# Kernel optimization log

Hardware: AMD Instinct MI355X
Metric: run time of the kernel (lower is better)

Reference implementation:

```python
import jax, jax.numpy as jnp
import numpy as np

D_MODEL = 1024
H = 16
T = 1024
B = 8

def setup_inputs() -> dict:
    key = jax.random.key(0)
    k0, k1, k2, k3, k4 = jax.random.split(key, 5)
    return {
        "x": jax.random.normal(k0, (B, T, D_MODEL), dtype=jnp.float32),
        "Wq": jax.random.normal(k1, (D_MODEL, D_MODEL), dtype=jnp.float32),
        "Wk": jax.random.normal(k2, (D_MODEL, D_MODEL), dtype=jnp.float32),
        "Wv": jax.random.normal(k3, (D_MODEL, D_MODEL), dtype=jnp.float32),
        "Wp": jax.random.normal(k4, (D_MODEL, D_MODEL), dtype=jnp.float32),
    }

def reference(x, Wq, Wk, Wv, Wp):
    b, t, d = x.shape
    dh = d // H
    # projections
    q = (x @ Wq).reshape(b, t, H, dh)
    k = (x @ Wk).reshape(b, t, H, dh)
    v = (x @ Wv).reshape(b, t, H, dh)
    # [b, h, t, t] attention scores, scaled by sqrt(d_head)
    scores = jnp.einsum("bqhd,bkhd->bhqk", q, k) / jnp.sqrt(jnp.float32(dh))
    attn = jax.nn.softmax(scores, axis=-1)
    # [b, h, t, dh] -> [b, t, d]
    out = jnp.einsum("bhqk,bkhd->bqhd", attn, v).reshape(b, t, d)
    return out @ Wp
```

## Files before the change

kernel.cpp:

```cpp
#include <hip/hip_runtime.h>
#include <math.h>


typedef unsigned short u16;
typedef unsigned int u32;
typedef __bf16  bf16x8 __attribute__((ext_vector_type(8)));
typedef unsigned short u16x8 __attribute__((ext_vector_type(8)));
typedef unsigned short u16x4 __attribute__((ext_vector_type(4)));
typedef short s16x4 __attribute__((ext_vector_type(4)));
typedef unsigned int u32x2 __attribute__((ext_vector_type(2)));
typedef float f32x4 __attribute__((ext_vector_type(4)));

#define MFMA16(a,b,c) __builtin_amdgcn_mfma_f32_16x16x32_bf16((a),(b),(c),0,0,0)
#define MFMA16K16(a,b,c) __builtin_amdgcn_mfma_f32_16x16x16bf16_1k((a),(b),(c),0,0,0)

static __device__ __forceinline__ u16 f2b(float f){
  unsigned u = __builtin_bit_cast(unsigned, f);
  u += 0x7fffu + ((u >> 16) & 1u);
  return (u16)(u >> 16);
}
static __device__ __forceinline__ float b2f(u16 h){
  unsigned u = ((unsigned)h) << 16;
  return __builtin_bit_cast(float, u);
}
static __device__ __forceinline__ bf16x8 ldsfrag(const u16* p){
  return __builtin_bit_cast(bf16x8, *(const u16x8*)p);
}
static __device__ __forceinline__ u32 packhi(float fa, float fb){
  return __builtin_amdgcn_perm(__builtin_bit_cast(u32, fa),
                               __builtin_bit_cast(u32, fb), 0x07060302u);
}
static __device__ __forceinline__ void gld16(const void* g, void* l){
  __builtin_amdgcn_global_load_lds(
      (const __attribute__((address_space(1))) void*)g,
      (__attribute__((address_space(3))) void*)l, 16, 0, 0);
}


__global__ __launch_bounds__(256) void split_x_kernel(
    const float* __restrict__ x, u16* __restrict__ xh, u16* __restrict__ xl, int n)
{
  int i = (blockIdx.x * 256 + threadIdx.x) * 8;
  if (i >= n) return;
  float4 v0 = *(const float4*)(x + i);
  float4 v1 = *(const float4*)(x + i + 4);
  float vv[8] = {v0.x, v0.y, v0.z, v0.w, v1.x, v1.y, v1.z, v1.w};
  u16x8 hv, lv;
#pragma unroll
  for (int j = 0; j < 8; j++){
    u16 hb = f2b(vv[j]);
    hv[j] = hb;
    lv[j] = f2b(vv[j] - b2f(hb));
  }
  *(u16x8*)(xh + i) = hv;
  *(u16x8*)(xl + i) = lv;
}

__global__ __launch_bounds__(256) void transpose4_kernel(
    const float* __restrict__ Wq, const float* __restrict__ Wk,
    const float* __restrict__ Wv, const float* __restrict__ Wp,
    u16* __restrict__ qh_, u16* __restrict__ ql_,
    u16* __restrict__ kh_, u16* __restrict__ kl_,
    u16* __restrict__ vt_, u16* __restrict__ pt_)
{
  __shared__ float t[32][33];
  const int z = blockIdx.z;
  const float* W = (z == 0) ? Wq : (z == 1) ? Wk : (z == 2) ? Wv : Wp;
  u16* Th = (z == 0) ? qh_ : (z == 1) ? kh_ : (z == 2) ? vt_ : pt_;
  u16* Tl = (z == 0) ? ql_ : (z == 1) ? kl_ : nullptr;
  int n0 = blockIdx.x * 32, k0 = blockIdx.y * 32;
  int tx = threadIdx.x, ty = threadIdx.y;
#pragma unroll
  for (int i = 0; i < 4; i++){
    int k = k0 + ty + i * 8;
    t[ty + i * 8][tx] = W[(size_t)k * 1024 + n0 + tx];
  }
  __syncthreads();
#pragma unroll
  for (int i = 0; i < 4; i++){
    int n = n0 + ty + i * 8;
    float v = t[tx][ty + i * 8];
    u16 h = f2b(v);
    Th[(size_t)n * 1024 + k0 + tx] = h;
    if (Tl) Tl[(size_t)n * 1024 + k0 + tx] = f2b(v - b2f(h));
  }
}

template<int OUTMODE>
__global__ __launch_bounds__(256) void gemm_bt_kernel(
    const u16* __restrict__ A, const u16* __restrict__ Bt, void* __restrict__ Cv,
    int M, int N, int K)
{
  __shared__ __attribute__((aligned(16))) u16 lA[4096], lB[4096];
  const int tid = threadIdx.x, lane = tid & 63, wave = tid >> 6;
  const int quad = lane >> 4, l15 = lane & 15;
  const int row0 = blockIdx.x * 128, col0 = blockIdx.y * 128;
  const int wm = wave >> 1, wn = wave & 1;
  const int sr = lane >> 2, sc = (lane & 3) * 8;
  f32x4 acc[4][4];
#pragma unroll
  for (int mt = 0; mt < 4; mt++)
#pragma unroll
    for (int nt = 0; nt < 4; nt++) acc[mt][nt] = (f32x4)0.0f;

  for (int k0 = 0; k0 < K; k0 += 32){
#pragma unroll
    for (int i = 0; i < 2; i++){
      int c = wave * 2 + i;
      gld16(A  + (size_t)(row0 + c * 16 + sr) * K + k0 + sc, &lA[c * 512]);
      gld16(Bt + (size_t)(col0 + c * 16 + sr) * K + k0 + sc, &lB[c * 512]);
    }
    __syncthreads();
    bf16x8 a[4], b[4];
#pragma unroll
    for (int t = 0; t < 4; t++){
      a[t] = ldsfrag(&lA[(wm * 64 + t * 16 + l15) * 32 + quad * 8]);
      b[t] = ldsfrag(&lB[(wn * 64 + t * 16 + l15) * 32 + quad * 8]);
    }
#pragma unroll
    for (int mt = 0; mt < 4; mt++)
#pragma unroll
      for (int nt = 0; nt < 4; nt++)
        acc[mt][nt] = MFMA16(a[mt], b[nt], acc[mt][nt]);
    __syncthreads();
  }
  if (OUTMODE == 2){
#pragma unroll
    for (int mt = 0; mt < 4; mt++)
#pragma unroll
      for (int nt = 0; nt < 4; nt++){
        int row = row0 + wm * 64 + mt * 16 + quad * 4;
        int col = col0 + wn * 64 + nt * 16 + l15;
        int bb = row >> 10, tt = row & 1023;
        int hh = (col >> 6) & 15, d = col & 63;
        int bhI = bb * 16 + hh;
        int ktile = tt >> 7, fkt = (tt >> 4) & 7, qF = (tt >> 2) & 3;
        int nd = d >> 4, l15F = d & 15;
        size_t idx = ((((size_t)(bhI * 8 + ktile) * 8 + fkt) * 4 + nd) * 64
                      + qF * 16 + l15F) * 4;
        u16x4 vals;
#pragma unroll
        for (int r = 0; r < 4; r++) vals[r] = f2b(acc[mt][nt][r]);
        *(u16x4*)(((u16*)Cv) + idx) = vals;
      }
  } else {
#pragma unroll
    for (int mt = 0; mt < 4; mt++)
#pragma unroll
      for (int nt = 0; nt < 4; nt++)
#pragma unroll
        for (int r = 0; r < 4; r++){
          int row = row0 + wm * 64 + mt * 16 + quad * 4 + r;
          int col = col0 + wn * 64 + nt * 16 + l15;
          ((float*)Cv)[(size_t)row * N + col] = acc[mt][nt][r];
        }
  }
}

__global__ __launch_bounds__(512, 2) void gemm_qk_kernel(
    const u16* __restrict__ Ah, const u16* __restrict__ Al,
    const u16* __restrict__ Bh, const u16* __restrict__ Bl,
    u16* __restrict__ Qhf, u16* __restrict__ Qlf,
    u16* __restrict__ Khf, u16* __restrict__ Klf, int M, int N, int K)
{
  __shared__ __attribute__((aligned(16))) u16 sA[2][2][8192], sB[2][2][8192];
  const int tid = threadIdx.x, lane = tid & 63, wave = tid >> 6;
  const int quad = lane >> 4, l15 = lane & 15;
  const int wm = wave >> 2, wn = wave & 3;
  const int row0 = blockIdx.x * 256, col0 = blockIdx.y * 256;
  const int f0a = (wave & 3) | ((wave & 4) << 1);
  const int f0b = (wave & 1) | ((wave >> 1) << 2);
  const size_t fstride = (size_t)16 * K;
  const size_t abase = (size_t)(row0 + l15) * K + quad * 8;
  const size_t bbase = (size_t)(col0 + l15) * K + quad * 8;
  (void)M; (void)N;

  f32x4 acc[8][4];
#pragma unroll
  for (int mt = 0; mt < 8; mt++)
#pragma unroll
    for (int nt = 0; nt < 4; nt++) acc[mt][nt] = (f32x4)0.0f;

#define STAGE_G0(KK, NB) do {                                              \
    gld16(Ah + abase + (size_t)f0a * fstride + (KK), &sA[NB][0][f0a * 512]); \
    gld16(Al + abase + (size_t)f0a * fstride + (KK), &sA[NB][1][f0a * 512]); \
    gld16(Bh + bbase + (size_t)f0b * fstride + (KK), &sB[NB][0][f0b * 512]); \
    gld16(Bl + bbase + (size_t)f0b * fstride + (KK), &sB[NB][1][f0b * 512]); \
  } while (0)
#define STAGE_G1(KK, NB) do {                                                        \
    gld16(Bh + bbase + (size_t)(f0b + 2) * fstride + (KK), &sB[NB][0][(f0b + 2) * 512]); \
    gld16(Bl + bbase + (size_t)(f0b + 2) * fstride + (KK), &sB[NB][1][(f0b + 2) * 512]); \
  } while (0)
#define STAGE_G2(KK, NB) do {                                                        \
    gld16(Ah + abase + (size_t)(f0a + 4) * fstride + (KK), &sA[NB][0][(f0a + 4) * 512]); \
    gld16(Al + abase + (size_t)(f0a + 4) * fstride + (KK), &sA[NB][1][(f0a + 4) * 512]); \
  } while (0)
#define RD_A(B4, BUF) do {                                        \
    _Pragma("unroll")                                             \
    for (int i = 0; i < 4; i++){                                  \
      int fa = wm * 8 + (B4) + i;                                 \
      ahf[i] = ldsfrag(&sA[BUF][0][fa * 512 + lane * 8]);         \
      alf[i] = ldsfrag(&sA[BUF][1][fa * 512 + lane * 8]);         \
    } } while (0)
#define RD_B(B2, BUF) do {                                        \
    _Pragma("unroll")                                             \
    for (int j = 0; j < 2; j++){                                  \
      int fb = wn * 4 + (B2) + j;                                 \
      bhf[j] = ldsfrag(&sB[BUF][0][fb * 512 + lane * 8]);         \
      blf[j] = ldsfrag(&sB[BUF][1][fb * 512 + lane * 8]);         \
    } } while (0)
#define MM(M0, N0) do {                                                      \
    __builtin_amdgcn_s_setprio(1);                                           \
    _Pragma("unroll")                                                        \
    for (int i = 0; i < 4; i++)                                              \
      _Pragma("unroll")                                                      \
      for (int j = 0; j < 2; j++){                                           \
        acc[(M0) + i][(N0) + j] = MFMA16(alf[i], bhf[j], acc[(M0) + i][(N0) + j]); \
        acc[(M0) + i][(N0) + j] = MFMA16(ahf[i], blf[j], acc[(M0) + i][(N0) + j]); \
        acc[(M0) + i][(N0) + j] = MFMA16(ahf[i], bhf[j], acc[(M0) + i][(N0) + j]); \
      }                                                                      \
    __builtin_amdgcn_s_setprio(0);                                           \
  } while (0)
#define VMCNT4() asm volatile("s_waitcnt vmcnt(4)" ::: "memory")
#define VMCNT6() asm volatile("s_waitcnt vmcnt(6)" ::: "memory")
#define BARRIER() asm volatile("s_barrier" ::: "memory")

  const int NT = K >> 5;
  STAGE_G0(0, 0);
  STAGE_G1(0, 0);
  STAGE_G2(0, 0);

  bf16x8 ahf[4], alf[4], bhf[2], blf[2];
#pragma unroll 2
  for (int t = 0; t < NT; t++){
    const int buf = t & 1, nb = buf ^ 1;
    const int kn = ((t + 1) & (NT - 1)) * 32;
    VMCNT4();
    BARRIER();
    RD_A(0, buf);
    RD_B(0, buf);
    STAGE_G0(kn, nb);
    MM(0, 0);
    VMCNT6();
    BARRIER();
    RD_B(2, buf);
    STAGE_G1(kn, nb);
    MM(0, 2);
    VMCNT6();
    BARRIER();
    RD_A(4, buf);
    STAGE_G2(kn, nb);
    MM(4, 2);
    RD_B(0, buf);
    MM(4, 0);
  }
  asm volatile("s_waitcnt vmcnt(0)" ::: "memory");

#undef STAGE_G0
#undef STAGE_G1
#undef STAGE_G2
#undef RD_A
#undef RD_B
#undef MM
#undef VMCNT4
#undef VMCNT6
#undef BARRIER

  const bool isQ = (col0 < 1024);
#pragma unroll
  for (int mt = 0; mt < 8; mt++)
#pragma unroll
    for (int nt = 0; nt < 4; nt++)
#pragma unroll
      for (int r = 0; r < 4; r++){
        int row = row0 + wm * 128 + mt * 16 + quad * 4 + r;
        int col = col0 + wn * 64 + nt * 16 + l15;
        int bb = row >> 10, tt = row & 1023;
        int hh = (col >> 6) & 15, d = col & 63;
        int bhI = bb * 16 + hh;
        int kc = d >> 5, qF = (d >> 3) & 3, j = d & 7;
        float v = acc[mt][nt][r];
        u16 hi = f2b(v);
        u16 lo = f2b(v - b2f(hi));
        if (isQ){
          int qtile = tt >> 7, rr = tt & 127;
          int wv = rr >> 5, mtF = (rr >> 4) & 1, l15F = tt & 15;
          size_t idx = ((((size_t)(bhI * 8 + qtile) * 4 + wv) * 2 + mtF) * 2 + kc) * 512
                       + (qF * 16 + l15F) * 8 + j;
          Qhf[idx] = hi; Qlf[idx] = lo;
        } else {
          int ktile = tt >> 7, fkt = (tt >> 4) & 7, l15F = tt & 15;
          size_t idx = (((size_t)(bhI * 8 + ktile) * 8 + fkt) * 2 + kc) * 512
                       + (qF * 16 + l15F) * 8 + j;
          Khf[idx] = hi; Klf[idx] = lo;
        }
      }
}

__global__ __launch_bounds__(256, 2) void attn_kernel(
    const u16* __restrict__ Qhf, const u16* __restrict__ Qlf,
    const u16* __restrict__ Khf, const u16* __restrict__ Klf,
    const u16* __restrict__ Vf, u16* __restrict__ O)
{
  __shared__ __attribute__((aligned(16))) u16 lKh[2][4096], lKl[2][4096], lV[2][4096];
  const int tid = threadIdx.x, lane = tid & 63, wave = tid >> 6;
  const int quad = lane >> 4, l15 = lane & 15;
  const int qt = blockIdx.x >> 7, bh = blockIdx.x & 127;
  const int b = bh >> 4, h = bh & 15;
  const int q0 = qt * 256;
  const float BETA = 0.18033688011112042f;

  bf16x8 qh[2][2][2], ql[2][2][2];
  {
    u16* sh = &lKh[0][0];  u16* sl = &lKl[0][0];
#pragma unroll
    for (int g = 0; g < 2; g++){
      size_t qbase = ((size_t)((bh * 8 + 2 * qt + g) * 4 + wave)) * 2048 + lane * 8;
#pragma unroll
      for (int i = 0; i < 4; i++){
        gld16(Qhf + qbase + i * 512, sh + wave * 2048 + i * 512);
        gld16(Qlf + qbase + i * 512, sl + wave * 2048 + i * 512);
      }
      __syncthreads();
#pragma unroll
      for (int mt = 0; mt < 2; mt++)
#pragma unroll
        for (int kc = 0; kc < 2; kc++){
          int off = wave * 2048 + (mt * 2 + kc) * 512 + lane * 8;
          qh[g][mt][kc] = ldsfrag(sh + off);
          ql[g][mt][kc] = ldsfrag(sl + off);
        }
      __syncthreads();
    }
  }

  float m_i[2][2] = {{-3.0e38f, -3.0e38f}, {-3.0e38f, -3.0e38f}};
  float l_i[2][2] = {{0.0f, 0.0f}, {0.0f, 0.0f}};
  f32x4 o_acc[2][2][4];
#pragma unroll
  for (int g = 0; g < 2; g++)
#pragma unroll
    for (int mt = 0; mt < 2; mt++)
#pragma unroll
      for (int nd = 0; nd < 4; nd++) o_acc[g][mt][nd] = (f32x4)0.0f;

  const size_t pan = (size_t)bh * 65536;
#pragma unroll
  for (int i = 0; i < 2; i++){
    int c = wave * 2 + i;
    gld16(Khf + pan + c * 512 + lane * 8, &lKh[0][c * 512]);
    gld16(Klf + pan + c * 512 + lane * 8, &lKl[0][c * 512]);
    gld16(Vf  + pan + c * 512 + lane * 8, &lV [0][c * 512]);
  }

#pragma unroll 1
  for (int j = 0; j < 16; j++){
    const int cur = j & 1;
    __syncthreads();
    if (j < 15){
      size_t nb = pan + (size_t)(j + 1) * 4096;
      const int nxt = cur ^ 1;
#pragma unroll
      for (int i = 0; i < 2; i++){
        int c = wave * 2 + i;
        gld16(Khf + nb + c * 512 + lane * 8, &lKh[nxt][c * 512]);
        gld16(Klf + nb + c * 512 + lane * 8, &lKl[nxt][c * 512]);
        gld16(Vf  + nb + c * 512 + lane * 8, &lV [nxt][c * 512]);
      }
    }

#pragma unroll
    for (int g = 0; g < 2; g++){
      f32x4 s[2][4];
#pragma unroll
      for (int qt2 = 0; qt2 < 2; qt2++)
#pragma unroll
        for (int f4 = 0; f4 < 4; f4++) s[qt2][f4] = (f32x4)0.0f;
#pragma unroll
      for (int f4 = 0; f4 < 4; f4++){
        int aoff = f4 * 1024 + lane * 8;
        bf16x8 kh0 = ldsfrag(&lKh[cur][aoff]);
        bf16x8 kh1 = ldsfrag(&lKh[cur][aoff + 512]);
        bf16x8 kl0 = ldsfrag(&lKl[cur][aoff]);
        bf16x8 kl1 = ldsfrag(&lKl[cur][aoff + 512]);
        __builtin_amdgcn_s_setprio(1);
#pragma unroll
        for (int qt2 = 0; qt2 < 2; qt2++){
          s[qt2][f4] = MFMA16(kl0, qh[g][qt2][0], s[qt2][f4]);
          s[qt2][f4] = MFMA16(kl1, qh[g][qt2][1], s[qt2][f4]);
          s[qt2][f4] = MFMA16(kh0, ql[g][qt2][0], s[qt2][f4]);
          s[qt2][f4] = MFMA16(kh1, ql[g][qt2][1], s[qt2][f4]);
          s[qt2][f4] = MFMA16(kh0, qh[g][qt2][0], s[qt2][f4]);
          s[qt2][f4] = MFMA16(kh1, qh[g][qt2][1], s[qt2][f4]);
        }
        __builtin_amdgcn_s_setprio(0);
      }

      float alpha[2];
#pragma unroll
      for (int qt2 = 0; qt2 < 2; qt2++){
        f32x4 mv = s[qt2][0];
#pragma unroll
        for (int f4 = 1; f4 < 4; f4++){
          mv[0] = fmaxf(mv[0], s[qt2][f4][0]); mv[1] = fmaxf(mv[1], s[qt2][f4][1]);
          mv[2] = fmaxf(mv[2], s[qt2][f4][2]); mv[3] = fmaxf(mv[3], s[qt2][f4][3]);
        }
        float mx = fmaxf(fmaxf(mv[0], mv[1]), fmaxf(mv[2], mv[3]));
        mx = fmaxf(mx, __shfl_xor(mx, 16));
        mx = fmaxf(mx, __shfl_xor(mx, 32));
        float mn = fmaxf(m_i[g][qt2], mx);
        alpha[qt2] = __builtin_amdgcn_exp2f((m_i[g][qt2] - mn) * BETA);
        m_i[g][qt2] = mn;
        float mb = mn * BETA;
        f32x4 ps = (f32x4)0.0f;
#pragma unroll
        for (int f4 = 0; f4 < 4; f4++)
#pragma unroll
          for (int r = 0; r < 4; r++){
            float p = __builtin_amdgcn_exp2f(s[qt2][f4][r] * BETA - mb);
            s[qt2][f4][r] = p;
            ps[r] += p;
          }
        float rs = (ps[0] + ps[1]) + (ps[2] + ps[3]);
        rs += __shfl_xor(rs, 16);
        rs += __shfl_xor(rs, 32);
        l_i[g][qt2] = l_i[g][qt2] * alpha[qt2] + rs;
      }

#pragma unroll
      for (int mt = 0; mt < 2; mt++)
#pragma unroll
        for (int r = 0; r < 4; r++){
          float ar = __shfl(alpha[mt], quad * 4 + r);
#pragma unroll
          for (int nd = 0; nd < 4; nd++) o_acc[g][mt][nd][r] *= ar;
        }

#pragma unroll
      for (int f4 = 0; f4 < 4; f4++){
        s16x4 vb[4];
#pragma unroll
        for (int nd = 0; nd < 4; nd++)
          vb[nd] = __builtin_bit_cast(s16x4,
                     *(const u16x4*)&lV[cur][(f4 * 4 + nd) * 256 + lane * 4]);
        __builtin_amdgcn_s_setprio(1);
#pragma unroll
        for (int qt2 = 0; qt2 < 2; qt2++){
          u32x2 pd;
          pd[0] = packhi(s[qt2][f4][1], s[qt2][f4][0]);
          pd[1] = packhi(s[qt2][f4][3], s[qt2][f4][2]);
          s16x4 pa = __builtin_bit_cast(s16x4, pd);
#pragma unroll
          for (int nd = 0; nd < 4; nd++)
            o_acc[g][qt2][nd] = MFMA16K16(pa, vb[nd], o_acc[g][qt2][nd]);
        }
        __builtin_amdgcn_s_setprio(0);
      }
    }
  }

#pragma unroll
  for (int g = 0; g < 2; g++)
#pragma unroll
    for (int mt = 0; mt < 2; mt++)
#pragma unroll
      for (int r = 0; r < 4; r++){
        float lr = __shfl(l_i[g][mt], quad * 4 + r);
        float inv = 1.0f / lr;
        int t = q0 + g * 128 + wave * 32 + mt * 16 + quad * 4 + r;
        size_t rowoff = (size_t)(b * 1024 + t) * 1024 + h * 64;
#pragma unroll
        for (int nd = 0; nd < 4; nd++)
          O[rowoff + nd * 16 + l15] = f2b(o_acc[g][mt][nd][r] * inv);
      }
}

extern "C" void kernel_launch(void* const* d_in, const int* in_sizes, int n_in,
                              void* d_out, int out_size, void* d_ws, size_t ws_size,
                              hipStream_t stream)
{
  const float* x  = (const float*)d_in[0];
  const float* Wq = (const float*)d_in[1];
  const float* Wk = (const float*)d_in[2];
  const float* Wv = (const float*)d_in[3];
  const float* Wp = (const float*)d_in[4];
  float* out = (float*)d_out;
  char* ws = (char*)d_ws;
  const size_t MB = 1024 * 1024;
  u16* xh   = (u16*)(ws + 0);
  u16* xl   = (u16*)(ws + 16 * MB);
  u16* wqkh = (u16*)(ws + 32 * MB);
  u16* wqkl = (u16*)(ws + 36 * MB);
  u16* wvt  = (u16*)(ws + 40 * MB);
  u16* wpt  = (u16*)(ws + 42 * MB);
  u16* Qhf  = (u16*)(ws + 44 * MB);
  u16* Qlf  = (u16*)(ws + 60 * MB);
  u16* Khf  = (u16*)(ws + 76 * MB);
  u16* Klf  = (u16*)(ws + 92 * MB);
  u16* Vf   = (u16*)(ws + 108 * MB);
  u16* obuf = xh;
  (void)in_sizes; (void)n_in; (void)out_size; (void)ws_size;

  split_x_kernel<<<4096, 256, 0, stream>>>(x, xh, xl, 8 * 1024 * 1024);
  transpose4_kernel<<<dim3(32, 32, 4), dim3(32, 8), 0, stream>>>(
      Wq, Wk, Wv, Wp, wqkh, wqkl, wqkh + 1024 * 1024, wqkl + 1024 * 1024, wvt, wpt);
  gemm_qk_kernel<<<dim3(32, 8), 512, 0, stream>>>(xh, xl, wqkh, wqkl,
                                                  Qhf, Qlf, Khf, Klf, 8192, 2048, 1024);
  gemm_bt_kernel<2><<<dim3(64, 8), 256, 0, stream>>>(xh, wvt, (void*)Vf, 8192, 1024, 1024);
  attn_kernel<<<512, 256, 0, stream>>>(Qhf, Qlf, Khf, Klf, Vf, obuf);
  gemm_bt_kernel<0><<<dim3(64, 8), 256, 0, stream>>>(obuf, wpt, (void*)out, 8192, 1024, 1024);
}
```

Baseline: 334.8 us.

## Double-buffer GEMM LDS tiles and prefetch next K-slice during MFMA

The projection GEMM kernel now keeps two LDS buffers and issues global-to-LDS loads for the next K-slice before computing on the current one, replacing the two syncthreads per iteration with a single waitcnt plus barrier. The LDS layout changes to lane-major fragment order, so each lane reads its fragment contiguously. MFMA sections are wrapped in s_setprio to favour math issue. This doubles LDS use per block, which may lower occupancy, and the wrapped prefetch on the last iteration issues redundant loads.

```diff
diff --git a/kernel.cpp b/kernel.cpp
--- a/kernel.cpp
+++ b/kernel.cpp
@@ -91,39 +91,54 @@
     const u16* __restrict__ A, const u16* __restrict__ Bt, void* __restrict__ Cv,
     int M, int N, int K)
 {
-  __shared__ __attribute__((aligned(16))) u16 lA[4096], lB[4096];
+  __shared__ __attribute__((aligned(16))) u16 lA[2][4096], lB[2][4096];
   const int tid = threadIdx.x, lane = tid & 63, wave = tid >> 6;
   const int quad = lane >> 4, l15 = lane & 15;
   const int row0 = blockIdx.x * 128, col0 = blockIdx.y * 128;
   const int wm = wave >> 1, wn = wave & 1;
-  const int sr = lane >> 2, sc = (lane & 3) * 8;
+  const int c0 = wave * 2, c1 = wave * 2 + 1;
+  const size_t ar0 = (size_t)(row0 + c0 * 16 + l15) * K + quad * 8;
+  const size_t ar1 = (size_t)(row0 + c1 * 16 + l15) * K + quad * 8;
+  const size_t br0 = (size_t)(col0 + c0 * 16 + l15) * K + quad * 8;
+  const size_t br1 = (size_t)(col0 + c1 * 16 + l15) * K + quad * 8;
   f32x4 acc[4][4];
 #pragma unroll
   for (int mt = 0; mt < 4; mt++)
 #pragma unroll
     for (int nt = 0; nt < 4; nt++) acc[mt][nt] = (f32x4)0.0f;
 
-  for (int k0 = 0; k0 < K; k0 += 32){
-#pragma unroll
-    for (int i = 0; i < 2; i++){
-      int c = wave * 2 + i;
-      gld16(A  + (size_t)(row0 + c * 16 + sr) * K + k0 + sc, &lA[c * 512]);
-      gld16(Bt + (size_t)(col0 + c * 16 + sr) * K + k0 + sc, &lB[c * 512]);
+  const int NT = K >> 5;
+  gld16(A  + ar0, &lA[0][c0 * 512]);
+  gld16(A  + ar1, &lA[0][c1 * 512]);
+  gld16(Bt + br0, &lB[0][c0 * 512]);
+  gld16(Bt + br1, &lB[0][c1 * 512]);
+
+#pragma unroll 2
+  for (int t = 0; t < NT; t++){
+    const int buf = t & 1, nb = buf ^ 1;
+    const int kn = ((t + 1) & (NT - 1)) * 32;
+    asm volatile("s_waitcnt vmcnt(0)" ::: "memory");
+    asm volatile("s_barrier" ::: "memory");
+    gld16(A  + ar0 + kn, &lA[nb][c0 * 512]);
+    gld16(A  + ar1 + kn, &lA[nb][c1 * 512]);
+    gld16(Bt + br0 + kn, &lB[nb][c0 * 512]);
+    gld16(Bt + br1 + kn, &lB[nb][c1 * 512]);
+    bf16x8 a[4], b[4];
+#pragma unroll
+    for (int f = 0; f < 4; f++){
+      a[f] = ldsfrag(&lA[buf][(wm * 4 + f) * 512 + lane * 8]);
+      b[f] = ldsfrag(&lB[buf][(wn * 4 + f) * 512 + lane * 8]);
     }
-    __syncthreads();
-    bf16x8 a[4], b[4];
-#pragma unroll
-    for (int t = 0; t < 4; t++){
-      a[t] = ldsfrag(&lA[(wm * 64 + t * 16 + l15) * 32 + quad * 8]);
-      b[t] = ldsfrag(&lB[(wn * 64 + t * 16 + l15) * 32 + quad * 8]);
-    }
+    __builtin_amdgcn_s_setprio(1);
 #pragma unroll
     for (int mt = 0; mt < 4; mt++)
 #pragma unroll
       for (int nt = 0; nt < 4; nt++)
         acc[mt][nt] = MFMA16(a[mt], b[nt], acc[mt][nt]);
-    __syncthreads();
-  }
+    __builtin_amdgcn_s_setprio(0);
+  }
+  asm volatile("s_waitcnt vmcnt(0)" ::: "memory");
+
   if (OUTMODE == 2){
 #pragma unroll
     for (int mt = 0; mt < 4; mt++)
```

Result: slower. 349.6 us (+4.4%).

## Double-buffer gemm_bt with 128x256 tiles, async prefetch and MFMA priority

Applied to the files above, without the earlier changes.

Reworks the bf16 B-transposed GEMM used for the V projection and the output projection. The block tile grows to 128x256 with 512 threads. Global-to-LDS loads for the next 64-wide K slice go into a second LDS buffer while MFMAs run on the current one, synchronised with manual vmcnt waits and barriers in place of two __syncthreads per step. LDS now holds fragments in lane-contiguous order, and s_setprio raises wave priority around the MFMA bursts. The goal is to hide global load latency and halve barrier overhead, at the cost of about 96KB of LDS per block, which limits occupancy.

```diff
diff --git a/kernel.cpp b/kernel.cpp
--- a/kernel.cpp
+++ b/kernel.cpp
@@ -87,43 +87,66 @@
 }
 
 template<int OUTMODE>
-__global__ __launch_bounds__(256) void gemm_bt_kernel(
+__global__ __launch_bounds__(512, 2) void gemm_bt_kernel(
     const u16* __restrict__ A, const u16* __restrict__ Bt, void* __restrict__ Cv,
     int M, int N, int K)
 {
-  __shared__ __attribute__((aligned(16))) u16 lA[4096], lB[4096];
+  __shared__ __attribute__((aligned(16))) u16 sA[2][2][4096], sB[2][2][8192];
   const int tid = threadIdx.x, lane = tid & 63, wave = tid >> 6;
   const int quad = lane >> 4, l15 = lane & 15;
-  const int row0 = blockIdx.x * 128, col0 = blockIdx.y * 128;
-  const int wm = wave >> 1, wn = wave & 1;
-  const int sr = lane >> 2, sc = (lane & 3) * 8;
+  const int wm = wave >> 2, wn = wave & 3;
+  const int row0 = blockIdx.x * 128, col0 = blockIdx.y * 256;
+  const size_t abase  = (size_t)(row0 + wave * 16 + l15) * K + quad * 8;
+  const size_t bbase0 = (size_t)(col0 + (2 * wave) * 16 + l15) * K + quad * 8;
+  const size_t bbase1 = (size_t)(col0 + (2 * wave + 1) * 16 + l15) * K + quad * 8;
+  (void)M;
+
   f32x4 acc[4][4];
 #pragma unroll
   for (int mt = 0; mt < 4; mt++)
 #pragma unroll
     for (int nt = 0; nt < 4; nt++) acc[mt][nt] = (f32x4)0.0f;
 
-  for (int k0 = 0; k0 < K; k0 += 32){
-#pragma unroll
-    for (int i = 0; i < 2; i++){
-      int c = wave * 2 + i;
-      gld16(A  + (size_t)(row0 + c * 16 + sr) * K + k0 + sc, &lA[c * 512]);
-      gld16(Bt + (size_t)(col0 + c * 16 + sr) * K + k0 + sc, &lB[c * 512]);
-    }
-    __syncthreads();
-    bf16x8 a[4], b[4];
-#pragma unroll
-    for (int t = 0; t < 4; t++){
-      a[t] = ldsfrag(&lA[(wm * 64 + t * 16 + l15) * 32 + quad * 8]);
-      b[t] = ldsfrag(&lB[(wn * 64 + t * 16 + l15) * 32 + quad * 8]);
-    }
-#pragma unroll
-    for (int mt = 0; mt < 4; mt++)
-#pragma unroll
-      for (int nt = 0; nt < 4; nt++)
-        acc[mt][nt] = MFMA16(a[mt], b[nt], acc[mt][nt]);
-    __syncthreads();
-  }
+#define BT_STAGE(C, KK, NB) do {                                           \
+    gld16(A  + abase  + (KK) + (C) * 32, &sA[NB][C][wave * 512]);          \
+    gld16(Bt + bbase0 + (KK) + (C) * 32, &sB[NB][C][(2 * wave) * 512]);    \
+    gld16(Bt + bbase1 + (KK) + (C) * 32, &sB[NB][C][(2 * wave + 1) * 512]);\
+  } while (0)
+#define BT_PHASE(C, BUF, KN, NB) do {                                      \
+    asm volatile("s_waitcnt vmcnt(3)" ::: "memory");                       \
+    asm volatile("s_barrier" ::: "memory");                                \
+    bf16x8 a[4], b[4];                                                     \
+    _Pragma("unroll")                                                      \
+    for (int f = 0; f < 4; f++){                                           \
+      a[f] = ldsfrag(&sA[BUF][C][(wm * 4 + f) * 512 + lane * 8]);          \
+      b[f] = ldsfrag(&sB[BUF][C][(wn * 4 + f) * 512 + lane * 8]);          \
+    }                                                                      \
+    BT_STAGE(C, KN, NB);                                                   \
+    __builtin_amdgcn_s_setprio(1);                                         \
+    _Pragma("unroll")                                                      \
+    for (int mt = 0; mt < 4; mt++)                                         \
+      _Pragma("unroll")                                                    \
+      for (int nt = 0; nt < 4; nt++)                                       \
+        acc[mt][nt] = MFMA16(a[mt], b[nt], acc[mt][nt]);                   \
+    __builtin_amdgcn_s_setprio(0);                                         \
+  } while (0)
+
+  const int NT = K >> 6;
+  BT_STAGE(0, 0, 0);
+  BT_STAGE(1, 0, 0);
+
+#pragma unroll 2
+  for (int t = 0; t < NT; t++){
+    const int buf = t & 1, nb = buf ^ 1;
+    const int kn = ((t + 1) & (NT - 1)) * 64;
+    BT_PHASE(0, buf, kn, nb);
+    BT_PHASE(1, buf, kn, nb);
+  }
+  asm volatile("s_waitcnt vmcnt(0)" ::: "memory");
+
+#undef BT_STAGE
+#undef BT_PHASE
+
   if (OUTMODE == 2){
 #pragma unroll
     for (int mt = 0; mt < 4; mt++)
@@ -506,7 +529,7 @@
       Wq, Wk, Wv, Wp, wqkh, wqkl, wqkh + 1024 * 1024, wqkl + 1024 * 1024, wvt, wpt);
   gemm_qk_kernel<<<dim3(32, 8), 512, 0, stream>>>(xh, xl, wqkh, wqkl,
                                                   Qhf, Qlf, Khf, Klf, 8192, 2048, 1024);
-  gemm_bt_kernel<2><<<dim3(64, 8), 256, 0, stream>>>(xh, wvt, (void*)Vf, 8192, 1024, 1024);
+  gemm_bt_kernel<2><<<dim3(64, 4), 512, 0, stream>>>(xh, wvt, (void*)Vf, 8192, 1024, 1024);
   attn_kernel<<<512, 256, 0, stream>>>(Qhf, Qlf, Khf, Klf, Vf, obuf);
-  gemm_bt_kernel<0><<<dim3(64, 8), 256, 0, stream>>>(obuf, wpt, (void*)out, 8192, 1024, 1024);
-}
+  gemm_bt_kernel<0><<<dim3(64, 4), 512, 0, stream>>>(obuf, wpt, (void*)out, 8192, 1024, 1024);
+}
```

Result: no change. 331.4 us (-1.0%).
